# Kernel optimization log

Measured on AMD Instinct MI355X. Metric: run time of the kernel, lower is better.

The kernel has to match this reference:

```python
import jax, jax.numpy as jnp
import numpy as np
import math

EMB = 128
KH = 256
VH = 256
NP_ = 32
B, T = 64, 1024


def setup_inputs() -> dict:
    key = jax.random.key(0)
    ks = jax.random.split(key, 12)
    s = 1.0 / math.sqrt(EMB)
    sk = 1.0 / math.sqrt(KH)
    return {
        "x": jax.random.normal(ks[0], (B, T, EMB), dtype=jnp.float32),
        "mask": jnp.ones((B, 1, T), dtype=bool),
        "person_idxs": jax.random.randint(ks[1], (B,), 0, NP_),
        # nn.Linear weights are [out, in]
        "Wk": jax.random.uniform(ks[2], (KH, EMB), jnp.float32, -s, s),
        "Wq": jax.random.uniform(ks[3], (KH, EMB), jnp.float32, -s, s),
        "Wv": jax.random.uniform(ks[4], (VH, EMB), jnp.float32, -s, s),
        # stacked per-person Linear(KH, KH) weights/biases (routing table)
        "PK_W": jax.random.uniform(ks[5], (NP_, KH, KH), jnp.float32, -sk, sk),
        "PK_b": jax.random.uniform(ks[6], (NP_, KH), jnp.float32, -sk, sk),
        "PQ_W": jax.random.uniform(ks[7], (NP_, KH, KH), jnp.float32, -sk, sk),
        "PQ_b": jax.random.uniform(ks[8], (NP_, KH), jnp.float32, -sk, sk),
    }


def reference(x, mask, person_idxs, Wk, Wq, Wv, PK_W, PK_b, PQ_W, PQ_b):
    # shared projections: [b,t,kh]
    k0 = jnp.einsum("bte,he->bth", x, Wk)
    q0 = jnp.einsum("bte,he->bth", x, Wq)
    v = jnp.einsum("bte,he->bth", x, Wv)  # [b,t,vh]
    # routed per-person linear: gather weights by person id, batched matmul
    keys = jnp.einsum("bth,boh->bto", k0, PK_W[person_idxs]) + PK_b[person_idxs][:, None, :]
    queries = jnp.einsum("bth,boh->bto", q0, PQ_W[person_idxs]) + PQ_b[person_idxs][:, None, :]
    queries = queries / math.sqrt(KH)
    dot = jnp.einsum("btd,bsd->bts", queries, keys)  # [b,t,t]
    dot = jnp.where(mask, dot, -jnp.inf)  # mask [b,1,t] broadcasts over query axis
    attention = jax.nn.softmax(dot, axis=-1)
    context = jnp.einsum("bts,bsd->btd", attention, v)  # [b,t,vh]
    return context
```

## Files before the change

### kernel.cpp

```cpp
#include <hip/hip_runtime.h>
#include <hip/hip_bf16.h>
#include <stdint.h>

#define EMB 128
#define KH  256
#define TT  1024

typedef __bf16 bf16x8 __attribute__((ext_vector_type(8)));
typedef float  f32x4  __attribute__((ext_vector_type(4)));
typedef float  f32x16 __attribute__((ext_vector_type(16)));
typedef unsigned short u16x8 __attribute__((ext_vector_type(8)));

__device__ inline unsigned short f2b(float f) {
  unsigned u = __builtin_bit_cast(unsigned, f);
  u += 0x7FFF + ((u >> 16) & 1);
  return (unsigned short)(u >> 16);
}

__device__ inline f32x4 mfma16(bf16x8 a, bf16x8 b, f32x4 c) {
  return __builtin_amdgcn_mfma_f32_16x16x32_bf16(a, b, c, 0, 0, 0);
}
__device__ inline f32x16 mfma32(bf16x8 a, bf16x8 b, f32x16 c) {
  return __builtin_amdgcn_mfma_f32_32x32x16_bf16(a, b, c, 0, 0, 0);
}
__device__ inline f32x16 zero16() {
  f32x16 z;
  #pragma unroll
  for (int i = 0; i < 16; ++i) z[i] = 0.f;
  return z;
}
__device__ inline void gload_lds16(const void* g, void* l) {
  __builtin_amdgcn_global_load_lds(
      (const __attribute__((address_space(1))) unsigned int*)g,
      (__attribute__((address_space(3))) unsigned int*)l, 16, 0, 0);
}

__global__ __launch_bounds__(256) void combine_kernel(
    const float* __restrict__ Wk, const float* __restrict__ Wq,
    const float* __restrict__ Wv,
    const float* __restrict__ PKW, const float* __restrict__ PQW,
    unsigned short* __restrict__ MK, unsigned short* __restrict__ MQ,
    unsigned short* __restrict__ Wvb)
{
  int bx = blockIdx.x;
  int tid = threadIdx.x;
  if (bx >= 256) {
    for (int i = tid; i < KH * EMB; i += 256) Wvb[i] = f2b(Wv[i]);
    return;
  }
  int mat = bx >> 7;
  int p   = (bx >> 2) & 31;
  int o0  = (bx & 3) * 64;
  const float* W  = mat ? Wq : Wk;
  const float* PW = (mat ? PQW : PKW) + (size_t)p * KH * KH;
  unsigned short* M = (mat ? MQ : MK) + (size_t)(p * KH + o0) * EMB;

  __shared__ float Wl[64 * 128];
  __shared__ float Pl[64 * 65];

  int e0 = (tid & 31) * 4;
  int og = tid >> 5;
  float acc[8][4] = {};

  for (int ht = 0; ht < KH; ht += 64) {
    __syncthreads();
    for (int i = tid; i < 64 * 128; i += 256)
      Wl[i] = W[(size_t)(ht + (i >> 7)) * EMB + (i & 127)];
    for (int i = tid; i < 64 * 64; i += 256) {
      int o = i >> 6, hh = i & 63;
      Pl[o * 65 + hh] = PW[(size_t)(o0 + o) * KH + ht + hh];
    }
    __syncthreads();
    for (int hh = 0; hh < 64; ++hh) {
      float4 wv4 = *(const float4*)&Wl[hh * 128 + e0];
      #pragma unroll
      for (int u = 0; u < 8; ++u) {
        float pv = Pl[(og + 8 * u) * 65 + hh];
        acc[u][0] += pv * wv4.x; acc[u][1] += pv * wv4.y;
        acc[u][2] += pv * wv4.z; acc[u][3] += pv * wv4.w;
      }
    }
  }
  float sc = mat ? 0.0625f : 1.0f;
  #pragma unroll
  for (int u = 0; u < 8; ++u) {
    int o = og + 8 * u;
    ushort4 st;
    st.x = f2b(acc[u][0] * sc); st.y = f2b(acc[u][1] * sc);
    st.z = f2b(acc[u][2] * sc); st.w = f2b(acc[u][3] * sc);
    *(ushort4*)&M[(size_t)o * EMB + e0] = st;
  }
}

__global__ __launch_bounds__(256) void proj_kernel(
    const float* __restrict__ x, const int* __restrict__ pidx,
    const unsigned short* __restrict__ MK, const unsigned short* __restrict__ MQ,
    const unsigned short* __restrict__ Wvb,
    const float* __restrict__ PKb, const float* __restrict__ PQb,
    unsigned short* __restrict__ Q, unsigned short* __restrict__ K,
    unsigned short* __restrict__ Vt)
{
  __shared__ unsigned short xl[64 * 128];
  __shared__ unsigned short vtl[4][4096];
  int b  = blockIdx.x >> 4;
  int t0 = (blockIdx.x & 15) * 64;
  int p  = pidx[b];
  int tid = threadIdx.x;

  for (int i = tid; i < 2048; i += 256) {
    int row = i >> 5, eg = i & 31;
    float4 v = *(const float4*)&x[(size_t)(b * TT + t0 + row) * EMB + eg * 4];
    int e = eg * 4;
    int sl = (e >> 3) ^ (row & 7);
    ushort4 s;
    s.x = f2b(v.x); s.y = f2b(v.y); s.z = f2b(v.z); s.w = f2b(v.w);
    *(ushort4*)&xl[row * 128 + sl * 8 + (e & 7)] = s;
  }
  __syncthreads();

  int w = tid >> 6, l = tid & 63, lr = l & 15, lg = l >> 4;

  bf16x8 a[4];
  {
    int row = 16 * w + lr;
    #pragma unroll
    for (int s = 0; s < 4; ++s) {
      int sl = (s * 4 + lg) ^ (row & 7);
      a[s] = *(const bf16x8*)&xl[row * 128 + sl * 8];
    }
  }

  #pragma unroll
  for (int mat = 0; mat < 2; ++mat) {
    const unsigned short* M = (mat ? MQ : MK) + (size_t)p * KH * EMB;
    const float* bias = (mat ? PQb : PKb) + (size_t)p * KH;
    unsigned short* Out = mat ? Q : K;
    float bscale = mat ? 0.0625f : 1.0f;
    f32x4 acc[16];
    #pragma unroll
    for (int i = 0; i < 16; ++i) acc[i] = (f32x4){0.f, 0.f, 0.f, 0.f};
    #pragma unroll
    for (int cf = 0; cf < 16; ++cf) {
      const unsigned short* Mp = M + (size_t)(cf * 16 + lr) * EMB + lg * 8;
      #pragma unroll
      for (int s = 0; s < 4; ++s) {
        bf16x8 bv = *(const bf16x8*)(Mp + 32 * s);
        acc[cf] = mfma16(a[s], bv, acc[cf]);
      }
    }
    unsigned short* vt = &vtl[w][0];
    #pragma unroll
    for (int cf = 0; cf < 16; ++cf) {
      int o = cf * 16 + lr;
      float bvv = bias[o] * bscale;
      int chunk = o >> 3;
      #pragma unroll
      for (int r = 0; r < 4; ++r) {
        int trow = lg * 4 + r;
        vt[trow * 256 + ((chunk ^ (trow & 7)) * 8) + (o & 7)] = f2b(acc[cf][r] + bvv);
      }
    }
    asm volatile("s_waitcnt lgkmcnt(0)" ::: "memory");
    __builtin_amdgcn_sched_barrier(0);
    int c = l & 31, rs = l >> 5;
    #pragma unroll
    for (int i = 0; i < 8; ++i) {
      int trow = i * 2 + rs;
      u16x8 v = *(const u16x8*)(vt + trow * 256 + c * 8);
      int g = c ^ (trow & 7);
      *(u16x8*)&Out[(size_t)(b * TT + t0 + w * 16 + trow) * KH + g * 8] = v;
    }
  }

  {
    f32x4 acc[16];
    #pragma unroll
    for (int i = 0; i < 16; ++i) acc[i] = (f32x4){0.f, 0.f, 0.f, 0.f};
    #pragma unroll
    for (int s = 0; s < 4; ++s) {
      bf16x8 bv[4];
      #pragma unroll
      for (int cf = 0; cf < 4; ++cf) {
        int row = cf * 16 + lr;
        int sl = (s * 4 + lg) ^ (row & 7);
        bv[cf] = *(const bf16x8*)&xl[row * 128 + sl * 8];
      }
      #pragma unroll
      for (int rf = 0; rf < 4; ++rf) {
        int d = 64 * w + rf * 16 + lr;
        bf16x8 av = *(const bf16x8*)&Wvb[(size_t)d * EMB + 32 * s + lg * 8];
        #pragma unroll
        for (int cf = 0; cf < 4; ++cf)
          acc[rf * 4 + cf] = mfma16(av, bv[cf], acc[rf * 4 + cf]);
      }
    }
    unsigned short* vt = &vtl[w][0];
    #pragma unroll
    for (int rf = 0; rf < 4; ++rf) {
      #pragma unroll
      for (int cf = 0; cf < 4; ++cf) {
        #pragma unroll
        for (int r = 0; r < 4; ++r) {
          int dl = rf * 16 + lg * 4 + r;
          int tc = cf * 16 + lr;
          int chunk = tc >> 3;
          vt[dl * 64 + ((chunk ^ (dl & 7)) * 8) + (tc & 7)] = f2b(acc[rf * 4 + cf][r]);
        }
      }
    }
    asm volatile("s_waitcnt lgkmcnt(0)" ::: "memory");
    __builtin_amdgcn_sched_barrier(0);
    int c8 = l & 7, r8 = l >> 3;
    #pragma unroll
    for (int i = 0; i < 8; ++i) {
      int dr = i * 8 + r8;
      u16x8 v = *(const u16x8*)(vt + dr * 64 + c8 * 8);
      int g = c8 ^ (dr & 7);
      *(u16x8*)&Vt[(size_t)(b * KH + w * 64 + dr) * TT + t0 + g * 8] = v;
    }
  }
}

__global__ __launch_bounds__(512, 2) void attn_kernel(
    const unsigned short* __restrict__ Q, const unsigned short* __restrict__ K,
    const unsigned short* __restrict__ Vt, float* __restrict__ out)
{
  __shared__ unsigned short Kl[2][64 * 256];
  __shared__ unsigned short Vl[2][32 * 256];
  __shared__ unsigned short Ptl[8][32 * 32];

  int bx = blockIdx.x;
  int slot = bx >> 3;
  int b  = (bx & 7) * 8 + (slot & 7);
  int qt = (slot >> 3) & 3;
  int dh = slot >> 5;

  int tid = threadIdx.x;
  int w = tid >> 6, l = tid & 63;
  int q31 = l & 31, h = l >> 5;

  const unsigned short* Kg = K + (size_t)b * TT * KH;
  const unsigned short* Vg = Vt + (size_t)(b * KH + dh * 128) * TT;
  int qbase = qt * 256 + w * 32;

  bf16x8 qa[16];
  {
    const unsigned short* Qp = Q + (size_t)(b * TT + qbase + q31) * KH + h * 8;
    #pragma unroll
    for (int s = 0; s < 16; ++s) qa[s] = *(const bf16x8*)(Qp + s * 16);
  }

  f32x16 acc[4];
  #pragma unroll
  for (int i = 0; i < 4; ++i) acc[i] = zero16();
  float psum[16];
  #pragma unroll
  for (int i = 0; i < 16; ++i) psum[i] = 0.f;

  auto stage = [&](int sb, int k0) {
    #pragma unroll
    for (int i = 0; i < 4; ++i) {
      int m = (w * 4 + i) * 64 + l;
      int row = m >> 5;
      int c = (m & 31) ^ (row & 31);
      gload_lds16(Kg + (size_t)(k0 + row) * KH + c * 8,
                  &Kl[sb][(w * 4 + i) * 512]);
    }
    #pragma unroll
    for (int i = 0; i < 2; ++i) {
      int m = (w * 2 + i) * 64 + l;
      int row = m >> 5;
      int u = (m & 31) ^ (row & 31);
      int dt = u >> 3, c = u & 7;
      gload_lds16(Vg + (size_t)(dt * 32 + row) * TT + k0 + c * 8,
                  &Vl[sb][(w * 2 + i) * 512]);
    }
  };

  stage(0, 0);
  unsigned short* myp = &Ptl[w][0];

  for (int kt = 0; kt < 16; ++kt) {
    int cur = kt & 1;
    if (kt < 15) {
      stage(cur ^ 1, (kt + 1) * 64);
      asm volatile("s_waitcnt vmcnt(6)" ::: "memory");
    } else {
      asm volatile("s_waitcnt vmcnt(0)" ::: "memory");
    }
    __builtin_amdgcn_s_barrier();
    __builtin_amdgcn_sched_barrier(0);
    const unsigned short* Kc = &Kl[cur][0];
    const unsigned short* Vc = &Vl[cur][0];

    #pragma unroll
    for (int kh = 0; kh < 2; ++kh) {
      f32x16 st = zero16();
      #pragma unroll
      for (int s = 0; s < 16; ++s) {
        bf16x8 kb = *(const bf16x8*)(Kc + (kh * 32 + q31) * 256 +
                                     (((2 * s + h) ^ q31) << 3));
        st = mfma32(qa[s], kb, st);
      }
      #pragma unroll
      for (int r = 0; r < 16; ++r) {
        float p = __expf(st[r]);
        psum[r] += p;
        int row = (r & 3) + 8 * (r >> 2) + 4 * h;
        int sl = (q31 >> 3) ^ (row & 3);
        myp[row * 32 + sl * 8 + (q31 & 7)] = f2b(p);
      }
      asm volatile("s_waitcnt lgkmcnt(0)" ::: "memory");
      __builtin_amdgcn_sched_barrier(0);
      #pragma unroll
      for (int s2 = 0; s2 < 2; ++s2) {
        bf16x8 pa = *(const bf16x8*)(myp + q31 * 32 +
                                     (((2 * s2 + h) ^ (q31 & 3)) << 3));
        #pragma unroll
        for (int dt = 0; dt < 4; ++dt) {
          int u = dt * 8 + 4 * kh + 2 * s2 + h;
          bf16x8 vb = *(const bf16x8*)(Vc + q31 * 256 + ((u ^ q31) << 3));
          acc[dt] = mfma32(pa, vb, acc[dt]);
        }
      }
    }
    __builtin_amdgcn_s_barrier();
    __builtin_amdgcn_sched_barrier(0);
  }

  #pragma unroll
  for (int m = 1; m < 32; m <<= 1) {
    #pragma unroll
    for (int r = 0; r < 16; ++r)
      psum[r] += __shfl_xor(psum[r], m, 64);
  }

  float* ob = out + (size_t)(b * TT + qbase) * KH + dh * 128;
  #pragma unroll
  for (int r = 0; r < 16; ++r) {
    int kk = (r & 3) + 8 * (r >> 2) + 4 * h;
    float inv = 1.0f / psum[r];
    #pragma unroll
    for (int dt = 0; dt < 4; ++dt)
      ob[(size_t)kk * KH + dt * 32 + q31] = acc[dt][r] * inv;
  }
}

extern "C" void kernel_launch(void* const* d_in, const int* in_sizes, int n_in,
                              void* d_out, int out_size, void* d_ws, size_t ws_size,
                              hipStream_t stream) {
  (void)in_sizes; (void)n_in; (void)out_size; (void)ws_size;
  const float* x    = (const float*)d_in[0];
  const int*   pidx = (const int*)d_in[2];
  const float* Wk   = (const float*)d_in[3];
  const float* Wq   = (const float*)d_in[4];
  const float* Wv   = (const float*)d_in[5];
  const float* PKW  = (const float*)d_in[6];
  const float* PKb  = (const float*)d_in[7];
  const float* PQW  = (const float*)d_in[8];
  const float* PQb  = (const float*)d_in[9];
  float* out = (float*)d_out;

  char* ws = (char*)d_ws;
  unsigned short* MK  = (unsigned short*)(ws);
  unsigned short* MQ  = (unsigned short*)(ws + (2u << 20));
  unsigned short* Wvb = (unsigned short*)(ws + (4u << 20));
  unsigned short* Qb  = (unsigned short*)(ws + (8u << 20));
  unsigned short* Kb  = (unsigned short*)(ws + (40u << 20));
  unsigned short* Vt  = (unsigned short*)(ws + (72u << 20));

  combine_kernel<<<257, 256, 0, stream>>>(Wk, Wq, Wv, PKW, PQW, MK, MQ, Wvb);
  proj_kernel<<<1024, 256, 0, stream>>>(x, pidx, MK, MQ, Wvb, PKb, PQb, Qb, Kb, Vt);
  attn_kernel<<<512, 512, 0, stream>>>(Qb, Kb, Vt, out);
}
```

Measured before the change: 248.9 us.

## Software-pipeline QK and PV halves with double-buffered padded P tiles

Each key tile's two 32-key halves are now interleaved. The QK^T MFMAs for the second half are issued before the PV MFMAs of the first half, so the exp and LDS write/read of P can overlap with matrix work. The P staging buffer is doubled and its row stride padded from 32 to 34 elements to reduce LDS bank conflicts. s_setprio is raised around the MFMA blocks. This uses more LDS and registers (two score accumulators live at once). The padded stride also makes the 16-byte P reads only 4-byte aligned, which depends on unaligned LDS access being handled.

```diff
diff --git a/kernel.cpp b/kernel.cpp
--- a/kernel.cpp
+++ b/kernel.cpp
@@ -227,7 +227,7 @@
 {
   __shared__ unsigned short Kl[2][64 * 256];
   __shared__ unsigned short Vl[2][32 * 256];
-  __shared__ unsigned short Ptl[8][32 * 32];
+  __shared__ unsigned short Ptl[8][2 * 1088];
 
   int bx = blockIdx.x;
   int slot = bx >> 3;
@@ -293,37 +293,69 @@
     const unsigned short* Kc = &Kl[cur][0];
     const unsigned short* Vc = &Vl[cur][0];
 
-    #pragma unroll
-    for (int kh = 0; kh < 2; ++kh) {
-      f32x16 st = zero16();
-      #pragma unroll
-      for (int s = 0; s < 16; ++s) {
-        bf16x8 kb = *(const bf16x8*)(Kc + (kh * 32 + q31) * 256 +
-                                     (((2 * s + h) ^ q31) << 3));
-        st = mfma32(qa[s], kb, st);
-      }
-      #pragma unroll
-      for (int r = 0; r < 16; ++r) {
-        float p = __expf(st[r]);
-        psum[r] += p;
-        int row = (r & 3) + 8 * (r >> 2) + 4 * h;
-        int sl = (q31 >> 3) ^ (row & 3);
-        myp[row * 32 + sl * 8 + (q31 & 7)] = f2b(p);
-      }
-      asm volatile("s_waitcnt lgkmcnt(0)" ::: "memory");
-      __builtin_amdgcn_sched_barrier(0);
-      #pragma unroll
-      for (int s2 = 0; s2 < 2; ++s2) {
-        bf16x8 pa = *(const bf16x8*)(myp + q31 * 32 +
-                                     (((2 * s2 + h) ^ (q31 & 3)) << 3));
-        #pragma unroll
-        for (int dt = 0; dt < 4; ++dt) {
-          int u = dt * 8 + 4 * kh + 2 * s2 + h;
-          bf16x8 vb = *(const bf16x8*)(Vc + q31 * 256 + ((u ^ q31) << 3));
-          acc[dt] = mfma32(pa, vb, acc[dt]);
-        }
-      }
-    }
+    f32x16 st0 = zero16();
+    __builtin_amdgcn_s_setprio(1);
+    #pragma unroll
+    for (int s = 0; s < 16; ++s) {
+      bf16x8 kb = *(const bf16x8*)(Kc + q31 * 256 + (((2 * s + h) ^ q31) << 3));
+      st0 = mfma32(qa[s], kb, st0);
+    }
+    __builtin_amdgcn_s_setprio(0);
+    #pragma unroll
+    for (int r = 0; r < 16; ++r) {
+      float p = __expf(st0[r]);
+      psum[r] += p;
+      int row = (r & 3) + 8 * (r >> 2) + 4 * h;
+      int sl = (q31 >> 3) ^ (row & 3);
+      myp[row * 34 + sl * 8 + (q31 & 7)] = f2b(p);
+    }
+    f32x16 st1 = zero16();
+    __builtin_amdgcn_s_setprio(1);
+    #pragma unroll
+    for (int s = 0; s < 16; ++s) {
+      bf16x8 kb = *(const bf16x8*)(Kc + (32 + q31) * 256 +
+                                   (((2 * s + h) ^ q31) << 3));
+      st1 = mfma32(qa[s], kb, st1);
+    }
+    __builtin_amdgcn_s_setprio(0);
+    asm volatile("s_waitcnt lgkmcnt(0)" ::: "memory");
+    __builtin_amdgcn_sched_barrier(0);
+    __builtin_amdgcn_s_setprio(1);
+    #pragma unroll
+    for (int s2 = 0; s2 < 2; ++s2) {
+      bf16x8 pa = *(const bf16x8*)(myp + q31 * 34 +
+                                   (((2 * s2 + h) ^ (q31 & 3)) << 3));
+      #pragma unroll
+      for (int dt = 0; dt < 4; ++dt) {
+        int u = dt * 8 + 2 * s2 + h;
+        bf16x8 vb = *(const bf16x8*)(Vc + q31 * 256 + ((u ^ q31) << 3));
+        acc[dt] = mfma32(pa, vb, acc[dt]);
+      }
+    }
+    __builtin_amdgcn_s_setprio(0);
+    #pragma unroll
+    for (int r = 0; r < 16; ++r) {
+      float p = __expf(st1[r]);
+      psum[r] += p;
+      int row = (r & 3) + 8 * (r >> 2) + 4 * h;
+      int sl = (q31 >> 3) ^ (row & 3);
+      myp[1088 + row * 34 + sl * 8 + (q31 & 7)] = f2b(p);
+    }
+    asm volatile("s_waitcnt lgkmcnt(0)" ::: "memory");
+    __builtin_amdgcn_sched_barrier(0);
+    __builtin_amdgcn_s_setprio(1);
+    #pragma unroll
+    for (int s2 = 0; s2 < 2; ++s2) {
+      bf16x8 pa = *(const bf16x8*)(myp + 1088 + q31 * 34 +
+                                   (((2 * s2 + h) ^ (q31 & 3)) << 3));
+      #pragma unroll
+      for (int dt = 0; dt < 4; ++dt) {
+        int u = dt * 8 + 4 + 2 * s2 + h;
+        bf16x8 vb = *(const bf16x8*)(Vc + q31 * 256 + ((u ^ q31) << 3));
+        acc[dt] = mfma32(pa, vb, acc[dt]);
+      }
+    }
+    __builtin_amdgcn_s_setprio(0);
     __builtin_amdgcn_s_barrier();
     __builtin_amdgcn_sched_barrier(0);
   }
```

Measured after the change: 258.1 us. 1.04x slower.
